# Optimization experiments

Hardware: AMD Instinct MI355X
Metric: run time of the kernel (lower is better)

The kernel has to match this reference:

```python
import jax, jax.numpy as jnp
import numpy as np

B, S, HID, H = 8, 128, 256, 4
DH = HID // H
FF = 4 * HID


def setup_inputs() -> dict:
    key = jax.random.key(0)
    ks = jax.random.split(key, 16)
    n = lambda i, shape: jax.random.normal(ks[i], shape, dtype=jnp.float32) * 0.02
    z = lambda shape: jnp.zeros(shape, dtype=jnp.float32)
    return dict(
        x=jax.random.normal(ks[0], (B, S, HID), dtype=jnp.float32),
        attention_mask=jnp.zeros((B, 1, S, S), dtype=jnp.float32),
        Wq=n(1, (HID, HID)), bq=z((HID,)),
        Wk=n(2, (HID, HID)), bk=z((HID,)),
        Wv=n(3, (HID, HID)), bv=z((HID,)),
        order_w=n(4, (2 * DH,)), order_b=z(()),
        dist_w=n(5, (2 * DH,)), dist_b=z(()),
        scalar=jax.random.normal(ks[6], (1,), dtype=jnp.float32),
        AWq=n(7, (HID, HID)), Abq=z((HID,)),
        AWk=n(8, (HID, HID)), Abk=z((HID,)),
        Wd=n(9, (HID, HID)), bd=z((HID,)),
        g1=jnp.ones((HID,), jnp.float32), beta1=z((HID,)),
        W1=n(10, (HID, FF)), b1=z((FF,)),
        W2=n(11, (FF, HID)), b2=z((HID,)),
        g2=jnp.ones((HID,), jnp.float32), beta2=z((HID,)),
    )


def _ln(t, g, b, eps=1e-12):
    m = t.mean(-1, keepdims=True)
    v = ((t - m) ** 2).mean(-1, keepdims=True)
    return (t - m) / jnp.sqrt(v + eps) * g + b


def _heads(t):
    # [B,S,HID] -> [B,H,S,DH]
    return t.reshape(B, S, H, DH).transpose(0, 2, 1, 3)


def reference(x, attention_mask, Wq, bq, Wk, bk, Wv, bv, order_w, order_b,
              dist_w, dist_b, scalar, AWq, Abq, AWk, Abk, Wd, bd,
              g1, beta1, W1, b1, W2, b2, g2, beta2):
    inv = 1.0 / jnp.sqrt(jnp.float32(DH))
    q = x @ Wq + bq
    k = x @ Wk + bk
    v = x @ Wv + bv
    qh, kh, vh = _heads(q), _heads(k), _heads(v)
    scores = jnp.einsum('bhqd,bhkd->bhqk', qh, kh)  # [B,H,S,S]

    # order/distance affines on concat(q_i, k_j): Linear(2*DH,1) decomposes into
    # per-token projections summed via broadcast (same math, no [B,H,S,S,2*DH] tensor)
    pr_order = jax.nn.sigmoid((qh @ order_w[:DH])[..., :, None]
                              + (kh @ order_w[DH:])[..., None, :] + order_b)
    gd_order = jnp.triu(jnp.ones((S, S), jnp.float32), k=1)
    err_order = (jnp.log(pr_order + 1e-24) * gd_order
                 + jnp.log(1.0 - pr_order + 1e-24) * (1.0 - gd_order))

    idx = jnp.arange(S)
    gd_dist = jnp.log(jnp.abs(idx[None, :] - idx[:, None]).astype(jnp.float32) + 1.0)
    pr_dist = ((qh @ dist_w[:DH])[..., :, None]
               + (kh @ dist_w[DH:])[..., None, :] + dist_b)
    err_dist = -jnp.square(gd_dist - pr_dist) * jnp.square(scalar[0]) * 0.5

    rich_scores = scores + err_order + err_dist
    softm = lambda s: jax.nn.softmax(s * inv + attention_mask, axis=-1)
    rich_probs = softm(rich_scores)
    origin_probs = softm(scores)

    # rich/calibrated combine ('fixed'): softmax(origin + 0.5 * rich)
    combined = jax.nn.softmax(origin_probs + 0.5 * rich_probs, axis=-1)

    # two-level attack attention on transformed mixed q/k
    aq, ak = _heads(q @ AWq + Abq), _heads(k @ AWk + Abk)
    attack_probs = softm(jnp.einsum('bhqd,bhkd->bhqk', aq, ak))
    final_probs = jax.nn.softmax(combined + 0.5 * attack_probs, axis=-1)

    ctx = jnp.einsum('bhqk,bhkd->bhqd', final_probs, vh)
    ctx = ctx.transpose(0, 2, 1, 3).reshape(B, S, HID)
    h = _ln(ctx @ Wd + bd + x, g1, beta1)
    f = jax.nn.gelu(h @ W1 + b1, approximate=False) @ W2 + b2
    return _ln(f + h, g2, beta2)
```

## Files before the change

kernel.cpp:

```cpp
#include <hip/hip_runtime.h>
#include <math.h>

#define B_  8
#define S_  128
#define HID_ 256
#define H_  4
#define DH_ 64
#define FF_ 1024
#define M_  (B_ * S_)

typedef _Float16 half_t;
typedef __attribute__((ext_vector_type(8))) _Float16 half8;
typedef __attribute__((ext_vector_type(4))) float floatx4;

enum { EP_F32 = 0, EP_F16 = 1, EP_F16B = 2, EP_GELU = 3, EP_PROJ = 4 };

__device__ __forceinline__ floatx4 mfma16(half8 a, half8 b, floatx4 c) {
    return __builtin_amdgcn_mfma_f32_16x16x32_f16(a, b, c, 0, 0, 0);
}

__device__ __forceinline__ float qred_sum(float v) {
#pragma unroll
    for (int o = 1; o < 16; o <<= 1) v += __shfl_xor(v, o, 64);
    return v;
}
__device__ __forceinline__ void sm8(float (&v)[8]) {
    float s = 0.f;
#pragma unroll
    for (int j = 0; j < 8; ++j) { v[j] = __expf(v[j]); s += v[j]; }
    s = qred_sum(s);
    float r = 1.f / s;
#pragma unroll
    for (int j = 0; j < 8; ++j) v[j] *= r;
}

template<int EPI, int KLEN>
__device__ __forceinline__ void mgemm(
    half8 (&Asf)[2][4][64], half8 (&Bsf)[2][4][64],
    const half_t* __restrict__ A, int ldA,
    const half_t* __restrict__ Bt, int ldB,
    int m0, int n0,
    const float* __restrict__ bias,
    float* __restrict__ Cf, half_t* __restrict__ Ch, int ldC,
    const float* __restrict__ pw1, const float* __restrict__ pw2,
    float* __restrict__ po1, float* __restrict__ po2, int hsel,
    int crb, int cnb, int tidp)
{
    constexpr int kt = KLEN >> 5;
    const int w = tidp >> 6, l = tidp & 63;
    const int sr = tidp >> 2;
    const int sq = tidp & 3;
    const int sdst = (sr & 15) | (sq << 4);
    const int smt = sr >> 4;
    const half_t* Ap = A + (size_t)(m0 + sr) * ldA + sq * 8;
    const half_t* Bp = Bt + (size_t)(n0 + sr) * ldB + sq * 8;

    half8 ra[kt], rb[kt];
#pragma unroll
    for (int t = 0; t < kt; ++t) {
        ra[t] = *(const half8*)(Ap + t * 32);
        rb[t] = *(const half8*)(Bp + t * 32);
    }

    floatx4 zero = {0.f, 0.f, 0.f, 0.f};
    floatx4 acc[4] = {zero, zero, zero, zero};

    Asf[0][smt][sdst] = ra[0];
    Bsf[0][smt][sdst] = rb[0];
    __syncthreads();
#pragma unroll
    for (int t = 0; t < kt; ++t) {
        const int buf = t & 1;
        half8 a = Asf[buf][w][l];
        acc[0] = mfma16(a, Bsf[buf][0][l], acc[0]);
        acc[1] = mfma16(a, Bsf[buf][1][l], acc[1]);
        acc[2] = mfma16(a, Bsf[buf][2][l], acc[2]);
        acc[3] = mfma16(a, Bsf[buf][3][l], acc[3]);
        if (t + 1 < kt) {
            Asf[buf ^ 1][smt][sdst] = ra[t + 1];
            Bsf[buf ^ 1][smt][sdst] = rb[t + 1];
            __syncthreads();
        }
    }

    const int quad = l >> 4, lc = l & 15;
    const int rowb = m0 + w * 16 + quad * 4;
    float bvv[4] = {0.f, 0.f, 0.f, 0.f};
    if (EPI >= EP_F16B) {
#pragma unroll
        for (int nt = 0; nt < 4; ++nt) bvv[nt] = bias[n0 + nt * 16 + lc];
    }
    float pw1v[4], pw2v[4];
    if (EPI == EP_PROJ) {
#pragma unroll
        for (int nt = 0; nt < 4; ++nt) {
            pw1v[nt] = pw1[nt * 16 + lc];
            pw2v[nt] = pw2[nt * 16 + lc];
        }
    }
#pragma unroll
    for (int rr = 0; rr < 4; ++rr) {
        float ov[4];
#pragma unroll
        for (int nt = 0; nt < 4; ++nt) {
            float o = acc[nt][rr];
            if (EPI >= EP_F16B) o += bvv[nt];
            if (EPI == EP_GELU) o = 0.5f * o * (1.f + erff(o * 0.70710678118654752f));
            ov[nt] = o;
            const size_t ci = (size_t)(rowb + rr - crb) * ldC + (n0 - cnb) + nt * 16 + lc;
            if (EPI == EP_F32) Cf[ci] = o;
            else Ch[ci] = (half_t)o;
        }
        if (EPI == EP_PROJ) {
            float po = ov[0] * pw1v[0] + ov[1] * pw1v[1] + ov[2] * pw1v[2] + ov[3] * pw1v[3];
            float pd = ov[0] * pw2v[0] + ov[1] * pw2v[1] + ov[2] * pw2v[2] + ov[3] * pw2v[3];
#pragma unroll
            for (int off = 1; off < 16; off <<= 1) {
                po += __shfl_xor(po, off, 64);
                pd += __shfl_xor(pd, off, 64);
            }
            if (lc == 0) {
                const int m = rowb + rr;
                const int idx = ((m >> 7) * H_ + hsel) * S_ + (m & 127);
                po1[idx] = po;
                po2[idx] = pd;
            }
        }
    }
}

__global__ __launch_bounds__(256) void prep_kernel(
    const float* __restrict__ x,
    const float* __restrict__ Wq, const float* __restrict__ Wk,
    const float* __restrict__ Wv, const float* __restrict__ Wd,
    const float* __restrict__ AWq, const float* __restrict__ AWk,
    const float* __restrict__ W1, const float* __restrict__ W2,
    half_t* __restrict__ x16, half_t* __restrict__ WqT, half_t* __restrict__ WkT,
    half_t* __restrict__ WvT, half_t* __restrict__ WdT,
    half_t* __restrict__ AWqT, half_t* __restrict__ AWkT,
    half_t* __restrict__ W1T, half_t* __restrict__ W2T)
{
    __shared__ half_t tl[64][72];
    const int tid = threadIdx.x;
    const int j = blockIdx.x;
    if (j < 256) {
        const int base = j * 1024 + tid * 4;
        float4 vv = *(const float4*)(x + base);
        x16[base + 0] = (half_t)vv.x;
        x16[base + 1] = (half_t)vv.y;
        x16[base + 2] = (half_t)vv.z;
        x16[base + 3] = (half_t)vv.w;
        return;
    }
    int t = j - 256;
    const float* src; half_t* dst; int K, N, k0, n0;
    if (t < 96) {
        int m = t >> 4, q = t & 15;
        const float* ins[6] = {Wq, Wk, Wv, Wd, AWq, AWk};
        half_t* outs[6] = {WqT, WkT, WvT, WdT, AWqT, AWkT};
        src = ins[m]; dst = outs[m]; K = 256; N = 256;
        k0 = (q & 3) * 64; n0 = (q >> 2) * 64;
    } else if (t < 160) {
        int q = t - 96; src = W1; dst = W1T; K = 256; N = 1024;
        k0 = (q & 3) * 64; n0 = (q >> 2) * 64;
    } else {
        int q = t - 160; src = W2; dst = W2T; K = 1024; N = 256;
        k0 = (q >> 2) * 64; n0 = (q & 3) * 64;
    }
    const int r = tid >> 2, c0 = (tid & 3) * 16;
#pragma unroll 4
    for (int i = 0; i < 16; ++i)
        tl[c0 + i][r] = (half_t)src[(size_t)(k0 + r) * N + n0 + c0 + i];
    __syncthreads();
#pragma unroll 4
    for (int i = 0; i < 16; ++i)
        dst[(size_t)(n0 + r) * K + k0 + c0 + i] = tl[r][c0 + i];
}

__global__ __launch_bounds__(256) void qkv_kernel(
    const half_t* __restrict__ x16,
    const half_t* __restrict__ WqT, const float* __restrict__ bq,
    const half_t* __restrict__ WkT, const float* __restrict__ bk,
    const half_t* __restrict__ WvT, const float* __restrict__ bv,
    const float* __restrict__ order_w, const float* __restrict__ dist_w,
    half_t* __restrict__ q16, half_t* __restrict__ k16, half_t* __restrict__ v16,
    float* __restrict__ qoA, float* __restrict__ qdA,
    float* __restrict__ koA, float* __restrict__ kdA)
{
    __shared__ half8 Asf[2][4][64], Bsf[2][4][64];
    const int j = blockIdx.x;
    const int z = j >> 6, q = j & 63;
    const int m0 = (q >> 2) * 64, n0 = (q & 3) * 64, bx = q & 3;
    if (z == 0)
        mgemm<EP_PROJ, 256>(Asf, Bsf, x16, HID_, WqT, HID_, m0, n0,
                            bq, nullptr, q16, HID_, order_w, dist_w, qoA, qdA, bx,
                            0, 0, threadIdx.x);
    else if (z == 1)
        mgemm<EP_PROJ, 256>(Asf, Bsf, x16, HID_, WkT, HID_, m0, n0,
                            bk, nullptr, k16, HID_, order_w + DH_, dist_w + DH_,
                            koA, kdA, bx, 0, 0, threadIdx.x);
    else
        mgemm<EP_F16B, 256>(Asf, Bsf, x16, HID_, WvT, HID_, m0, n0,
                            bv, nullptr, v16, HID_, nullptr, nullptr, nullptr, nullptr, 0,
                            0, 0, threadIdx.x);
}

struct AttnSmem {
    union {
        struct { half8 Asf[2][2][4][64]; half8 Bsf[2][2][4][64]; } g;
        struct { half_t Vt[64][136]; half8 Kf[2][8][64];
                 half_t Pm[8][16][136]; } a;
    } u;
    half_t aq_s[128][72];
    half_t ak_s[128][72];
};

__global__ __launch_bounds__(512) void attn_kernel(
    const half_t* __restrict__ q16, const half_t* __restrict__ k16,
    const half_t* __restrict__ v16,
    const half_t* __restrict__ AWqT, const half_t* __restrict__ AWkT,
    const float* __restrict__ Abq, const float* __restrict__ Abk,
    const float* __restrict__ qoA, const float* __restrict__ qdA,
    const float* __restrict__ koA, const float* __restrict__ kdA,
    const float* __restrict__ mask,
    const float* __restrict__ order_b_p, const float* __restrict__ dist_b_p,
    const float* __restrict__ scalar_p,
    half_t* __restrict__ ctx16)
{
    __shared__ AttnSmem sm;
    const int bh = blockIdx.x;
    const int b = bh >> 2, h = bh & 3;
    const int tid = threadIdx.x;
    const int half_id = tid >> 8, ltid = tid & 255;
    const int w = tid >> 6, l = tid & 63;
    const int quad = l >> 4, lc = l & 15;
    const size_t hoff = (size_t)b * S_ * HID_ + (size_t)h * DH_;
    const floatx4 zero = {0.f, 0.f, 0.f, 0.f};

    {
        const half_t* Asrc = half_id ? (k16 + (size_t)b * S_ * HID_)
                                     : (q16 + (size_t)b * S_ * HID_);
        const half_t* WT   = half_id ? AWkT : AWqT;
        const float*  bb   = half_id ? Abk : Abq;
        half_t* dst        = half_id ? &sm.ak_s[0][0] : &sm.aq_s[0][0];
        mgemm<EP_F16B, 256>(sm.u.g.Asf[half_id], sm.u.g.Bsf[half_id],
                            Asrc, HID_, WT, HID_, 0, h * DH_,
                            bb, nullptr, dst, 72, nullptr, nullptr, nullptr, nullptr, 0,
                            0, h * DH_, ltid);
        mgemm<EP_F16B, 256>(sm.u.g.Asf[half_id], sm.u.g.Bsf[half_id],
                            Asrc, HID_, WT, HID_, 64, h * DH_,
                            bb, nullptr, dst, 72, nullptr, nullptr, nullptr, nullptr, 0,
                            0, h * DH_, ltid);
    }
    __syncthreads();

#pragma unroll
    for (int u = 0; u < 2; ++u) {
        int idx = u * 512 + tid;
        int jj = idx >> 3, c = idx & 7;
        size_t g = hoff + (size_t)jj * HID_ + c * 8;
        int kt2 = c >> 2, jt = jj >> 4, sl = (jj & 15) | ((c & 3) << 4);
        sm.u.a.Kf[kt2][jt][sl] = *(const half8*)(k16 + g);
    }
#pragma unroll
    for (int u = 0; u < 2; ++u) {
        int idx = u * 512 + tid;
        int jj = idx >> 3, c = idx & 7;
        half8 vv = *(const half8*)(v16 + hoff + (size_t)jj * HID_ + c * 8);
#pragma unroll
        for (int e = 0; e < 8; ++e) sm.u.a.Vt[c * 8 + e][jj] = vv[e];
    }
    __syncthreads();

    const float ob = order_b_p[0], db = dist_b_p[0];
    const float scl = scalar_p[0];
    const float s2 = scl * scl;
    const float inv = 0.125f;
    float kov[8], kdv[8];
#pragma unroll
    for (int jt = 0; jt < 8; ++jt) {
        kov[jt] = koA[bh * S_ + jt * 16 + lc];
        kdv[jt] = kdA[bh * S_ + jt * 16 + lc];
    }

    const int rt = w;
    half8 qf[2], aqf[2];
#pragma unroll
    for (int kt = 0; kt < 2; ++kt) {
        qf[kt]  = *(const half8*)(q16 + hoff + (size_t)(rt * 16 + lc) * HID_
                                  + kt * 32 + quad * 8);
        aqf[kt] = *(const half8*)&sm.aq_s[rt * 16 + lc][kt * 32 + quad * 8];
    }
    floatx4 accS[8], accA[8];
#pragma unroll
    for (int jt = 0; jt < 8; ++jt) { accS[jt] = zero; accA[jt] = zero; }
#pragma unroll
    for (int kt = 0; kt < 2; ++kt) {
#pragma unroll
        for (int jt = 0; jt < 8; ++jt) {
            accS[jt] = mfma16(qf[kt], sm.u.a.Kf[kt][jt][l], accS[jt]);
            half8 bfr = *(const half8*)&sm.ak_s[jt * 16 + lc][kt * 32 + quad * 8];
            accA[jt] = mfma16(aqf[kt], bfr, accA[jt]);
        }
    }
#pragma unroll
    for (int reg = 0; reg < 4; ++reg) {
        const int il = quad * 4 + reg;
        const int i  = rt * 16 + il;
        float qo = qoA[bh * S_ + i], qd = qdA[bh * S_ + i];
        const float* mrow = mask + ((size_t)(b * S_ + i)) * S_;
        float mk[8], lg[8], as_[8];
#pragma unroll
        for (int jt = 0; jt < 8; ++jt) {
            mk[jt] = mrow[jt * 16 + lc];
            lg[jt] = accS[jt][reg];
            as_[jt] = accA[jt][reg];
        }
        float p0[8];
#pragma unroll
        for (int jt = 0; jt < 8; ++jt) p0[jt] = lg[jt] * inv + mk[jt];
        sm8(p0);
        float p1[8];
#pragma unroll
        for (int jt = 0; jt < 8; ++jt) {
            int j = jt * 16 + lc;
            float pr = 1.f / (1.f + __expf(-(qo + kov[jt] + ob)));
            float sel = (j > i) ? pr : 1.f - pr;
            float erro = __logf(sel + 1e-24f);
            float gd = __logf(fabsf((float)(j - i)) + 1.f);
            float dd = gd - (qd + kdv[jt] + db);
            p1[jt] = (lg[jt] + erro - 0.5f * dd * dd * s2) * inv + mk[jt];
        }
        sm8(p1);
#pragma unroll
        for (int jt = 0; jt < 8; ++jt) p0[jt] += 0.5f * p1[jt];
        sm8(p0);
#pragma unroll
        for (int jt = 0; jt < 8; ++jt) p1[jt] = as_[jt] * inv + mk[jt];
        sm8(p1);
#pragma unroll
        for (int jt = 0; jt < 8; ++jt) p0[jt] += 0.5f * p1[jt];
        sm8(p0);
#pragma unroll
        for (int jt = 0; jt < 8; ++jt) sm.u.a.Pm[w][il][jt * 16 + lc] = (half_t)p0[jt];
    }
    half8 pa_[4];
#pragma unroll
    for (int kt = 0; kt < 4; ++kt)
        pa_[kt] = *(const half8*)&sm.u.a.Pm[w][lc][kt * 32 + quad * 8];
    floatx4 apv[4] = {zero, zero, zero, zero};
#pragma unroll
    for (int nt = 0; nt < 4; ++nt) {
#pragma unroll
        for (int kt = 0; kt < 4; ++kt) {
            half8 vf = *(const half8*)&sm.u.a.Vt[nt * 16 + lc][kt * 32 + quad * 8];
            apv[nt] = mfma16(pa_[kt], vf, apv[nt]);
        }
    }
#pragma unroll
    for (int nt = 0; nt < 4; ++nt) {
#pragma unroll
        for (int reg = 0; reg < 4; ++reg) {
            int i = rt * 16 + quad * 4 + reg;
            ctx16[hoff + (size_t)i * HID_ + nt * 16 + lc] = (half_t)apv[nt][reg];
        }
    }
}

struct TailSmem {
    half8 Af[8][64];
    float hS[16][257];
    half_t h16L[16][264];
    half_t f116L[16][1032];
};

__global__ __launch_bounds__(512) void tail_kernel(
    const half_t* __restrict__ ctx16, const half_t* __restrict__ WdT,
    const float* __restrict__ x, const float* __restrict__ bd,
    const float* __restrict__ g1, const float* __restrict__ beta1,
    const half_t* __restrict__ W1T, const float* __restrict__ b1,
    const half_t* __restrict__ W2T, const float* __restrict__ b2,
    const float* __restrict__ g2, const float* __restrict__ beta2,
    float* __restrict__ out)
{
    __shared__ TailSmem sm;
    const int tid = threadIdx.x;
    const int r0 = blockIdx.x * 16;
    const int w = tid >> 6, l = tid & 63;
    const int quad = l >> 4, lc = l & 15;
    const floatx4 zero = {0.f, 0.f, 0.f, 0.f};

    {
        int row = tid >> 5, c = tid & 31;
        sm.Af[c >> 2][row | ((c & 3) << 4)] =
            *(const half8*)(ctx16 + (size_t)(r0 + row) * HID_ + c * 8);
    }
    __syncthreads();

    {
        const int n0 = w * 32;
        half8 bw[8][2];
#pragma unroll
        for (int kt = 0; kt < 8; ++kt)
#pragma unroll
            for (int nt = 0; nt < 2; ++nt)
                bw[kt][nt] = *(const half8*)(WdT + (size_t)(n0 + nt * 16 + lc) * HID_
                                             + kt * 32 + quad * 8);
        floatx4 acc[2] = {zero, zero};
#pragma unroll
        for (int kt = 0; kt < 8; ++kt) {
            half8 a = sm.Af[kt][l];
            acc[0] = mfma16(a, bw[kt][0], acc[0]);
            acc[1] = mfma16(a, bw[kt][1], acc[1]);
        }
#pragma unroll
        for (int nt = 0; nt < 2; ++nt)
#pragma unroll
            for (int rr = 0; rr < 4; ++rr) {
                int row = quad * 4 + rr, col = n0 + nt * 16 + lc;
                sm.hS[row][col] = acc[nt][rr] + bd[col]
                                + x[(size_t)(r0 + row) * HID_ + col];
            }
    }
    __syncthreads();

    {
        const int row = tid >> 5, jj = tid & 31;
        float s = 0.f;
#pragma unroll
        for (int i = 0; i < 8; ++i) s += sm.hS[row][i * 32 + jj];
#pragma unroll
        for (int o = 1; o < 32; o <<= 1) s += __shfl_xor(s, o, 64);
        float mean = s * (1.f / 256.f);
        float vs = 0.f;
#pragma unroll
        for (int i = 0; i < 8; ++i) { float d = sm.hS[row][i * 32 + jj] - mean; vs += d * d; }
#pragma unroll
        for (int o = 1; o < 32; o <<= 1) vs += __shfl_xor(vs, o, 64);
        float rs = rsqrtf(vs * (1.f / 256.f) + 1e-12f);
#pragma unroll
        for (int i = 0; i < 8; ++i) {
            int col = i * 32 + jj;
            float v = (sm.hS[row][col] - mean) * rs * g1[col] + beta1[col];
            sm.hS[row][col] = v;
            sm.h16L[row][col] = (half_t)v;
        }
    }
    __syncthreads();

#pragma unroll
    for (int nb = 0; nb < 2; ++nb) {
        const int n0 = w * 128 + nb * 64;
        floatx4 acc[4] = {zero, zero, zero, zero};
        half8 bw[2][4][4];
#pragma unroll
        for (int kt = 0; kt < 4; ++kt)
#pragma unroll
            for (int nt = 0; nt < 4; ++nt)
                bw[0][kt][nt] = *(const half8*)(W1T + (size_t)(n0 + nt * 16 + lc) * HID_
                                                + kt * 32 + quad * 8);
#pragma unroll
        for (int c = 0; c < 2; ++c) {
            if (c == 0) {
#pragma unroll
                for (int kt = 0; kt < 4; ++kt)
#pragma unroll
                    for (int nt = 0; nt < 4; ++nt)
                        bw[1][kt][nt] = *(const half8*)(W1T
                            + (size_t)(n0 + nt * 16 + lc) * HID_ + (4 + kt) * 32 + quad * 8);
            }
#pragma unroll
            for (int kt = 0; kt < 4; ++kt) {
                half8 a = *(const half8*)&sm.h16L[l & 15][(c * 4 + kt) * 32 + quad * 8];
#pragma unroll
                for (int nt = 0; nt < 4; ++nt)
                    acc[nt] = mfma16(a, bw[c][kt][nt], acc[nt]);
            }
        }
#pragma unroll
        for (int nt = 0; nt < 4; ++nt)
#pragma unroll
            for (int rr = 0; rr < 4; ++rr) {
                int row = quad * 4 + rr, col = n0 + nt * 16 + lc;
                float o = acc[nt][rr] + b1[col];
                o = 0.5f * o * (1.f + erff(o * 0.70710678118654752f));
                sm.f116L[row][col] = (half_t)o;
            }
    }
    __syncthreads();

    {
        const int n0 = w * 32;
        floatx4 acc[2] = {zero, zero};
        half8 bw[2][4][2];
#pragma unroll
        for (int kt = 0; kt < 4; ++kt)
#pragma unroll
            for (int nt = 0; nt < 2; ++nt)
                bw[0][kt][nt] = *(const half8*)(W2T + (size_t)(n0 + nt * 16 + lc) * FF_
                                                + kt * 32 + quad * 8);
#pragma unroll
        for (int c = 0; c < 8; ++c) {
            if (c < 7) {
#pragma unroll
                for (int kt = 0; kt < 4; ++kt)
#pragma unroll
                    for (int nt = 0; nt < 2; ++nt)
                        bw[(c + 1) & 1][kt][nt] = *(const half8*)(W2T
                            + (size_t)(n0 + nt * 16 + lc) * FF_ + ((c + 1) * 4 + kt) * 32 + quad * 8);
            }
#pragma unroll
            for (int kt = 0; kt < 4; ++kt) {
                half8 a = *(const half8*)&sm.f116L[l & 15][(c * 4 + kt) * 32 + quad * 8];
#pragma unroll
                for (int nt = 0; nt < 2; ++nt)
                    acc[nt] = mfma16(a, bw[c & 1][kt][nt], acc[nt]);
            }
        }
#pragma unroll
        for (int nt = 0; nt < 2; ++nt)
#pragma unroll
            for (int rr = 0; rr < 4; ++rr) {
                int row = quad * 4 + rr, col = n0 + nt * 16 + lc;
                sm.hS[row][col] = acc[nt][rr] + b2[col] + sm.hS[row][col];
            }
    }
    __syncthreads();

    {
        const int row = tid >> 5, jj = tid & 31;
        float s = 0.f;
#pragma unroll
        for (int i = 0; i < 8; ++i) s += sm.hS[row][i * 32 + jj];
#pragma unroll
        for (int o = 1; o < 32; o <<= 1) s += __shfl_xor(s, o, 64);
        float mean = s * (1.f / 256.f);
        float vs = 0.f;
#pragma unroll
        for (int i = 0; i < 8; ++i) { float d = sm.hS[row][i * 32 + jj] - mean; vs += d * d; }
#pragma unroll
        for (int o = 1; o < 32; o <<= 1) vs += __shfl_xor(vs, o, 64);
        float rs = rsqrtf(vs * (1.f / 256.f) + 1e-12f);
#pragma unroll
        for (int i = 0; i < 8; ++i) {
            int col = i * 32 + jj;
            out[(size_t)(r0 + row) * HID_ + col] =
                (sm.hS[row][col] - mean) * rs * g2[col] + beta2[col];
        }
    }
}

extern "C" void kernel_launch(void* const* d_in, const int* in_sizes, int n_in,
                              void* d_out, int out_size, void* d_ws, size_t ws_size,
                              hipStream_t stream) {
    const float* x        = (const float*)d_in[0];
    const float* mask     = (const float*)d_in[1];
    const float* Wq       = (const float*)d_in[2];
    const float* bq       = (const float*)d_in[3];
    const float* Wk       = (const float*)d_in[4];
    const float* bk       = (const float*)d_in[5];
    const float* Wv       = (const float*)d_in[6];
    const float* bv       = (const float*)d_in[7];
    const float* order_w  = (const float*)d_in[8];
    const float* order_b  = (const float*)d_in[9];
    const float* dist_w   = (const float*)d_in[10];
    const float* dist_b   = (const float*)d_in[11];
    const float* scalar   = (const float*)d_in[12];
    const float* AWq      = (const float*)d_in[13];
    const float* Abq      = (const float*)d_in[14];
    const float* AWk      = (const float*)d_in[15];
    const float* Abk      = (const float*)d_in[16];
    const float* Wd       = (const float*)d_in[17];
    const float* bd       = (const float*)d_in[18];
    const float* g1       = (const float*)d_in[19];
    const float* beta1    = (const float*)d_in[20];
    const float* W1       = (const float*)d_in[21];
    const float* b1       = (const float*)d_in[22];
    const float* W2       = (const float*)d_in[23];
    const float* b2       = (const float*)d_in[24];
    const float* g2       = (const float*)d_in[25];
    const float* beta2    = (const float*)d_in[26];

    float* ws = (float*)d_ws;
    size_t off = 0;
    auto ahf = [&](size_t nh) { half_t* p = (half_t*)(ws + off); off += nh / 2; return p; };
    auto afl = [&](size_t n) { float* p = ws + off; off += n; return p; };

    half_t* x16   = ahf(M_ * HID_);
    half_t* WqT   = ahf(HID_ * HID_);
    half_t* WkT   = ahf(HID_ * HID_);
    half_t* WvT   = ahf(HID_ * HID_);
    half_t* WdT   = ahf(HID_ * HID_);
    half_t* AWqT  = ahf(HID_ * HID_);
    half_t* AWkT  = ahf(HID_ * HID_);
    half_t* W1T   = ahf(HID_ * FF_);
    half_t* W2T   = ahf(HID_ * FF_);
    half_t* q16   = ahf(M_ * HID_);
    half_t* k16   = ahf(M_ * HID_);
    half_t* v16   = ahf(M_ * HID_);
    half_t* ctx16 = ahf(M_ * HID_);
    float* qoA  = afl(B_ * H_ * S_);
    float* qdA  = afl(B_ * H_ * S_);
    float* koA  = afl(B_ * H_ * S_);
    float* kdA  = afl(B_ * H_ * S_);

    prep_kernel<<<480, 256, 0, stream>>>(
        x, Wq, Wk, Wv, Wd, AWq, AWk, W1, W2,
        x16, WqT, WkT, WvT, WdT, AWqT, AWkT, W1T, W2T);
    qkv_kernel<<<192, 256, 0, stream>>>(
        x16, WqT, bq, WkT, bk, WvT, bv, order_w, dist_w,
        q16, k16, v16, qoA, qdA, koA, kdA);
    attn_kernel<<<32, 512, 0, stream>>>(
        q16, k16, v16, AWqT, AWkT, Abq, Abk,
        qoA, qdA, koA, kdA, mask, order_b, dist_b, scalar, ctx16);
    tail_kernel<<<64, 512, 0, stream>>>(
        ctx16, WdT, x, bd, g1, beta1, W1T, b1, W2T, b2, g2, beta2, (float*)d_out);
}
```

Baseline: 178.6 us.

## Defer late weight transposes into qkv kernel and restructure attack projection

Moves the transposes of Wd, AWq, AWk, W1 and W2 out of the prep kernel and into extra blocks of the qkv kernel, so the prep kernel only converts what the qkv GEMM needs and the remaining conversions run alongside the projection blocks. The attack projection in the attention kernel is also rebuilt: each block stages its head's AWq/AWk slice in shared memory, and every wave computes 16 rows of aq and ak with register-held q/k fragments, replacing the two chained mgemm calls per half-block. This shortens the critical path before the attention kernel starts and removes the staged-GEMM synchronisations. The cost is a larger shared-memory layout and more global reads of q16 and k16 in the attention kernel.

```diff
diff --git a/kernel.cpp b/kernel.cpp
--- a/kernel.cpp
+++ b/kernel.cpp
@@ -32,6 +32,20 @@
     float r = 1.f / s;
 #pragma unroll
     for (int j = 0; j < 8; ++j) v[j] *= r;
+}
+
+__device__ __forceinline__ void tr_tile(half_t (&tl)[64][72],
+    const float* __restrict__ src, half_t* __restrict__ dst,
+    int K, int N, int k0, int n0, int tid)
+{
+    const int r = tid >> 2, c0 = (tid & 3) * 16;
+#pragma unroll 4
+    for (int i = 0; i < 16; ++i)
+        tl[c0 + i][r] = (half_t)src[(size_t)(k0 + r) * N + n0 + c0 + i];
+    __syncthreads();
+#pragma unroll 4
+    for (int i = 0; i < 16; ++i)
+        dst[(size_t)(n0 + r) * K + k0 + c0 + i] = tl[r][c0 + i];
 }
 
 template<int EPI, int KLEN>
@@ -132,13 +146,9 @@
 __global__ __launch_bounds__(256) void prep_kernel(
     const float* __restrict__ x,
     const float* __restrict__ Wq, const float* __restrict__ Wk,
-    const float* __restrict__ Wv, const float* __restrict__ Wd,
-    const float* __restrict__ AWq, const float* __restrict__ AWk,
-    const float* __restrict__ W1, const float* __restrict__ W2,
+    const float* __restrict__ Wv,
     half_t* __restrict__ x16, half_t* __restrict__ WqT, half_t* __restrict__ WkT,
-    half_t* __restrict__ WvT, half_t* __restrict__ WdT,
-    half_t* __restrict__ AWqT, half_t* __restrict__ AWkT,
-    half_t* __restrict__ W1T, half_t* __restrict__ W2T)
+    half_t* __restrict__ WvT)
 {
     __shared__ half_t tl[64][72];
     const int tid = threadIdx.x;
@@ -153,28 +163,10 @@
         return;
     }
     int t = j - 256;
-    const float* src; half_t* dst; int K, N, k0, n0;
-    if (t < 96) {
-        int m = t >> 4, q = t & 15;
-        const float* ins[6] = {Wq, Wk, Wv, Wd, AWq, AWk};
-        half_t* outs[6] = {WqT, WkT, WvT, WdT, AWqT, AWkT};
-        src = ins[m]; dst = outs[m]; K = 256; N = 256;
-        k0 = (q & 3) * 64; n0 = (q >> 2) * 64;
-    } else if (t < 160) {
-        int q = t - 96; src = W1; dst = W1T; K = 256; N = 1024;
-        k0 = (q & 3) * 64; n0 = (q >> 2) * 64;
-    } else {
-        int q = t - 160; src = W2; dst = W2T; K = 1024; N = 256;
-        k0 = (q >> 2) * 64; n0 = (q & 3) * 64;
-    }
-    const int r = tid >> 2, c0 = (tid & 3) * 16;
-#pragma unroll 4
-    for (int i = 0; i < 16; ++i)
-        tl[c0 + i][r] = (half_t)src[(size_t)(k0 + r) * N + n0 + c0 + i];
-    __syncthreads();
-#pragma unroll 4
-    for (int i = 0; i < 16; ++i)
-        dst[(size_t)(n0 + r) * K + k0 + c0 + i] = tl[r][c0 + i];
+    int m = t >> 4, q = t & 15;
+    const float* ins[3] = {Wq, Wk, Wv};
+    half_t* outs[3] = {WqT, WkT, WvT};
+    tr_tile(tl, ins[m], outs[m], 256, 256, (q & 3) * 64, (q >> 2) * 64, tid);
 }
 
 __global__ __launch_bounds__(256) void qkv_kernel(
@@ -185,34 +177,62 @@
     const float* __restrict__ order_w, const float* __restrict__ dist_w,
     half_t* __restrict__ q16, half_t* __restrict__ k16, half_t* __restrict__ v16,
     float* __restrict__ qoA, float* __restrict__ qdA,
-    float* __restrict__ koA, float* __restrict__ kdA)
+    float* __restrict__ koA, float* __restrict__ kdA,
+    const float* __restrict__ Wd, const float* __restrict__ AWq,
+    const float* __restrict__ AWk, const float* __restrict__ W1,
+    const float* __restrict__ W2,
+    half_t* __restrict__ WdT, half_t* __restrict__ AWqT, half_t* __restrict__ AWkT,
+    half_t* __restrict__ W1T, half_t* __restrict__ W2T)
 {
-    __shared__ half8 Asf[2][4][64], Bsf[2][4][64];
+    __shared__ union {
+        struct { half8 Asf[2][4][64]; half8 Bsf[2][4][64]; } g;
+        half_t tl[64][72];
+    } sm;
     const int j = blockIdx.x;
-    const int z = j >> 6, q = j & 63;
-    const int m0 = (q >> 2) * 64, n0 = (q & 3) * 64, bx = q & 3;
-    if (z == 0)
-        mgemm<EP_PROJ, 256>(Asf, Bsf, x16, HID_, WqT, HID_, m0, n0,
-                            bq, nullptr, q16, HID_, order_w, dist_w, qoA, qdA, bx,
-                            0, 0, threadIdx.x);
-    else if (z == 1)
-        mgemm<EP_PROJ, 256>(Asf, Bsf, x16, HID_, WkT, HID_, m0, n0,
-                            bk, nullptr, k16, HID_, order_w + DH_, dist_w + DH_,
-                            koA, kdA, bx, 0, 0, threadIdx.x);
-    else
-        mgemm<EP_F16B, 256>(Asf, Bsf, x16, HID_, WvT, HID_, m0, n0,
-                            bv, nullptr, v16, HID_, nullptr, nullptr, nullptr, nullptr, 0,
-                            0, 0, threadIdx.x);
+    if (j < 192) {
+        const int z = j >> 6, q = j & 63;
+        const int m0 = (q >> 2) * 64, n0 = (q & 3) * 64, bx = q & 3;
+        if (z == 0)
+            mgemm<EP_PROJ, 256>(sm.g.Asf, sm.g.Bsf, x16, HID_, WqT, HID_, m0, n0,
+                                bq, nullptr, q16, HID_, order_w, dist_w, qoA, qdA, bx,
+                                0, 0, threadIdx.x);
+        else if (z == 1)
+            mgemm<EP_PROJ, 256>(sm.g.Asf, sm.g.Bsf, x16, HID_, WkT, HID_, m0, n0,
+                                bk, nullptr, k16, HID_, order_w + DH_, dist_w + DH_,
+                                koA, kdA, bx, 0, 0, threadIdx.x);
+        else
+            mgemm<EP_F16B, 256>(sm.g.Asf, sm.g.Bsf, x16, HID_, WvT, HID_, m0, n0,
+                                bv, nullptr, v16, HID_, nullptr, nullptr, nullptr, nullptr, 0,
+                                0, 0, threadIdx.x);
+        return;
+    }
+    int t = j - 192;
+    const float* src; half_t* dst; int K, N, k0, n0;
+    if (t < 48) {
+        int m = t >> 4, q = t & 15;
+        const float* ins[3] = {Wd, AWq, AWk};
+        half_t* outs[3] = {WdT, AWqT, AWkT};
+        src = ins[m]; dst = outs[m]; K = 256; N = 256;
+        k0 = (q & 3) * 64; n0 = (q >> 2) * 64;
+    } else if (t < 112) {
+        int q = t - 48; src = W1; dst = W1T; K = 256; N = 1024;
+        k0 = (q & 3) * 64; n0 = (q >> 2) * 64;
+    } else {
+        int q = t - 112; src = W2; dst = W2T; K = 1024; N = 256;
+        k0 = (q >> 2) * 64; n0 = (q & 3) * 64;
+    }
+    tr_tile(sm.tl, src, dst, K, N, k0, n0, threadIdx.x);
 }
 
 struct AttnSmem {
     union {
-        struct { half8 Asf[2][2][4][64]; half8 Bsf[2][2][4][64]; } g;
-        struct { half_t Vt[64][136]; half8 Kf[2][8][64];
-                 half_t Pm[8][16][136]; } a;
+        struct { half_t AWqS[64][264]; half_t AWkS[64][264]; } w;
+        half_t Pm[8][16][136];
     } u;
-    half_t aq_s[128][72];
+    half8 Kf[2][8][64];
+    half_t Vt[64][136];
     half_t ak_s[128][72];
+    half_t aq_s[8][16][72];
 };
 
 __global__ __launch_bounds__(512) void attn_kernel(
@@ -231,36 +251,30 @@
     const int bh = blockIdx.x;
     const int b = bh >> 2, h = bh & 3;
     const int tid = threadIdx.x;
-    const int half_id = tid >> 8, ltid = tid & 255;
     const int w = tid >> 6, l = tid & 63;
     const int quad = l >> 4, lc = l & 15;
     const size_t hoff = (size_t)b * S_ * HID_ + (size_t)h * DH_;
+    const size_t broff = (size_t)b * S_ * HID_;
     const floatx4 zero = {0.f, 0.f, 0.f, 0.f};
 
     {
-        const half_t* Asrc = half_id ? (k16 + (size_t)b * S_ * HID_)
-                                     : (q16 + (size_t)b * S_ * HID_);
-        const half_t* WT   = half_id ? AWkT : AWqT;
-        const float*  bb   = half_id ? Abk : Abq;
-        half_t* dst        = half_id ? &sm.ak_s[0][0] : &sm.aq_s[0][0];
-        mgemm<EP_F16B, 256>(sm.u.g.Asf[half_id], sm.u.g.Bsf[half_id],
-                            Asrc, HID_, WT, HID_, 0, h * DH_,
-                            bb, nullptr, dst, 72, nullptr, nullptr, nullptr, nullptr, 0,
-                            0, h * DH_, ltid);
-        mgemm<EP_F16B, 256>(sm.u.g.Asf[half_id], sm.u.g.Bsf[half_id],
-                            Asrc, HID_, WT, HID_, 64, h * DH_,
-                            bb, nullptr, dst, 72, nullptr, nullptr, nullptr, nullptr, 0,
-                            0, h * DH_, ltid);
-    }
-    __syncthreads();
-
+        const half_t* srcq = AWqT + (size_t)(h * DH_) * HID_;
+        const half_t* srck = AWkT + (size_t)(h * DH_) * HID_;
+        const int row = tid >> 5, c8 = (tid & 31) * 8;
+#pragma unroll
+        for (int p = 0; p < 4; ++p) {
+            int r = p * 16 + row;
+            *(half8*)&sm.u.w.AWqS[r][c8] = *(const half8*)(srcq + (size_t)r * HID_ + c8);
+            *(half8*)&sm.u.w.AWkS[r][c8] = *(const half8*)(srck + (size_t)r * HID_ + c8);
+        }
+    }
 #pragma unroll
     for (int u = 0; u < 2; ++u) {
         int idx = u * 512 + tid;
         int jj = idx >> 3, c = idx & 7;
         size_t g = hoff + (size_t)jj * HID_ + c * 8;
         int kt2 = c >> 2, jt = jj >> 4, sl = (jj & 15) | ((c & 3) << 4);
-        sm.u.a.Kf[kt2][jt][sl] = *(const half8*)(k16 + g);
+        sm.Kf[kt2][jt][sl] = *(const half8*)(k16 + g);
     }
 #pragma unroll
     for (int u = 0; u < 2; ++u) {
@@ -268,7 +282,40 @@
         int jj = idx >> 3, c = idx & 7;
         half8 vv = *(const half8*)(v16 + hoff + (size_t)jj * HID_ + c * 8);
 #pragma unroll
-        for (int e = 0; e < 8; ++e) sm.u.a.Vt[c * 8 + e][jj] = vv[e];
+        for (int e = 0; e < 8; ++e) sm.Vt[c * 8 + e][jj] = vv[e];
+    }
+    __syncthreads();
+
+    {
+        half8 qa[8], ka[8];
+#pragma unroll
+        for (int kt = 0; kt < 8; ++kt) {
+            size_t rq = broff + (size_t)(w * 16 + lc) * HID_ + kt * 32 + quad * 8;
+            qa[kt] = *(const half8*)(q16 + rq);
+            ka[kt] = *(const half8*)(k16 + rq);
+        }
+        floatx4 aacc[4] = {zero, zero, zero, zero};
+        floatx4 kacc[4] = {zero, zero, zero, zero};
+#pragma unroll
+        for (int kt = 0; kt < 8; ++kt) {
+#pragma unroll
+            for (int nt = 0; nt < 4; ++nt) {
+                half8 bq8 = *(const half8*)&sm.u.w.AWqS[nt * 16 + lc][kt * 32 + quad * 8];
+                half8 bk8 = *(const half8*)&sm.u.w.AWkS[nt * 16 + lc][kt * 32 + quad * 8];
+                aacc[nt] = mfma16(qa[kt], bq8, aacc[nt]);
+                kacc[nt] = mfma16(ka[kt], bk8, kacc[nt]);
+            }
+        }
+#pragma unroll
+        for (int nt = 0; nt < 4; ++nt) {
+            float bq_ = Abq[h * DH_ + nt * 16 + lc];
+            float bk_ = Abk[h * DH_ + nt * 16 + lc];
+#pragma unroll
+            for (int rr = 0; rr < 4; ++rr) {
+                sm.aq_s[w][quad * 4 + rr][nt * 16 + lc] = (half_t)(aacc[nt][rr] + bq_);
+                sm.ak_s[w * 16 + quad * 4 + rr][nt * 16 + lc] = (half_t)(kacc[nt][rr] + bk_);
+            }
+        }
     }
     __syncthreads();
 
@@ -289,7 +336,7 @@
     for (int kt = 0; kt < 2; ++kt) {
         qf[kt]  = *(const half8*)(q16 + hoff + (size_t)(rt * 16 + lc) * HID_
                                   + kt * 32 + quad * 8);
-        aqf[kt] = *(const half8*)&sm.aq_s[rt * 16 + lc][kt * 32 + quad * 8];
+        aqf[kt] = *(const half8*)&sm.aq_s[w][lc][kt * 32 + quad * 8];
     }
     floatx4 accS[8], accA[8];
 #pragma unroll
@@ -298,7 +345,7 @@
     for (int kt = 0; kt < 2; ++kt) {
 #pragma unroll
         for (int jt = 0; jt < 8; ++jt) {
-            accS[jt] = mfma16(qf[kt], sm.u.a.Kf[kt][jt][l], accS[jt]);
+            accS[jt] = mfma16(qf[kt], sm.Kf[kt][jt][l], accS[jt]);
             half8 bfr = *(const half8*)&sm.ak_s[jt * 16 + lc][kt * 32 + quad * 8];
             accA[jt] = mfma16(aqf[kt], bfr, accA[jt]);
         }
@@ -342,18 +389,18 @@
         for (int jt = 0; jt < 8; ++jt) p0[jt] += 0.5f * p1[jt];
         sm8(p0);
 #pragma unroll
-        for (int jt = 0; jt < 8; ++jt) sm.u.a.Pm[w][il][jt * 16 + lc] = (half_t)p0[jt];
+        for (int jt = 0; jt < 8; ++jt) sm.u.Pm[w][il][jt * 16 + lc] = (half_t)p0[jt];
     }
     half8 pa_[4];
 #pragma unroll
     for (int kt = 0; kt < 4; ++kt)
-        pa_[kt] = *(const half8*)&sm.u.a.Pm[w][lc][kt * 32 + quad * 8];
+        pa_[kt] = *(const half8*)&sm.u.Pm[w][lc][kt * 32 + quad * 8];
     floatx4 apv[4] = {zero, zero, zero, zero};
 #pragma unroll
     for (int nt = 0; nt < 4; ++nt) {
 #pragma unroll
         for (int kt = 0; kt < 4; ++kt) {
-            half8 vf = *(const half8*)&sm.u.a.Vt[nt * 16 + lc][kt * 32 + quad * 8];
+            half8 vf = *(const half8*)&sm.Vt[nt * 16 + lc][kt * 32 + quad * 8];
             apv[nt] = mfma16(pa_[kt], vf, apv[nt]);
         }
     }
@@ -604,12 +651,12 @@
     float* koA  = afl(B_ * H_ * S_);
     float* kdA  = afl(B_ * H_ * S_);
 
-    prep_kernel<<<480, 256, 0, stream>>>(
-        x, Wq, Wk, Wv, Wd, AWq, AWk, W1, W2,
-        x16, WqT, WkT, WvT, WdT, AWqT, AWkT, W1T, W2T);
-    qkv_kernel<<<192, 256, 0, stream>>>(
+    prep_kernel<<<304, 256, 0, stream>>>(
+        x, Wq, Wk, Wv, x16, WqT, WkT, WvT);
+    qkv_kernel<<<368, 256, 0, stream>>>(
         x16, WqT, bq, WkT, bk, WvT, bv, order_w, dist_w,
-        q16, k16, v16, qoA, qdA, koA, kdA);
+        q16, k16, v16, qoA, qdA, koA, kdA,
+        Wd, AWq, AWk, W1, W2, WdT, AWqT, AWkT, W1T, W2T);
     attn_kernel<<<32, 512, 0, stream>>>(
         q16, k16, v16, AWqT, AWkT, Abq, Abk,
         qoA, qdA, koA, kdA, mask, order_b, dist_b, scalar, ctx16);
```

Measured after the change: 174.4 us. 2.4% less time.
